# Performance work log

Measured on AMD Instinct MI355X. Metric: run time of the kernel, lower is better.

Reference implementation:

```python
import jax, jax.numpy as jnp
import numpy as np
from jax import lax

B, DIM, DIM_OUT, NH = 8, 512, 512, 8
HD = DIM_OUT // NH          # 64, also the depthwise-conv channel count
SQ, SKV = (1, 1), (2, 2)    # stride_q, stride_kv
PAD = 1                      # kernel 3 -> padding 3//2
SCALE = HD ** -0.5
EPS = 1e-6


def _dw_conv(x, w, stride):
    # x: [N, C, H, W], w: [C, 1, kh, kw]; depthwise conv (groups = C), no bias
    return lax.conv_general_dilated(
        x, w, window_strides=stride, padding=[(PAD, PAD), (PAD, PAD)],
        dimension_numbers=('NCHW', 'OIHW', 'NCHW'),
        feature_group_count=x.shape[1])


def _ln(x, w, b):
    m = jnp.mean(x, -1, keepdims=True)
    v = jnp.var(x, -1, keepdims=True)
    return (x - m) * lax.rsqrt(v + EPS) * w + b


def _pool(t, w, stride, ln_w, ln_b, H, W):
    # t: [B, NH, 1+H*W, HD] with cls token at index 0
    Bn = t.shape[0]
    cls = t[:, :, :1, :]
    body = t[:, :, 1:, :].reshape(Bn * NH, H, W, HD).transpose(0, 3, 1, 2)
    body = _dw_conv(body, w, stride)
    ph, pw = body.shape[2], body.shape[3]
    body = body.reshape(Bn, NH, HD, ph * pw).transpose(0, 1, 3, 2)
    out = jnp.concatenate([cls, body], axis=2)
    return _ln(out, ln_w, ln_b), (ph, pw)


def _rel_bias(r_q4, q_shape, k_shape, rel_pos_h, rel_pos_w):
    # r_q4: [B, NH, q_h*q_w, HD] (cls token stripped)
    q_h, q_w = q_shape
    k_h, k_w = k_shape

    def dist(qs, ks):
        qr, kr = max(ks / qs, 1.0), max(qs / ks, 1.0)
        d = np.arange(qs)[:, None] * qr - np.arange(ks)[None, :] * kr + (ks - 1) * kr
        return d.astype(np.int64)

    Rh = rel_pos_h[dist(q_h, k_h)]  # [q_h, k_h, HD]
    Rw = rel_pos_w[dist(q_w, k_w)]  # [q_w, k_w, HD]
    r_q = r_q4.reshape(r_q4.shape[0], NH, q_h, q_w, HD)
    rel_h = jnp.einsum('byhwc,hkc->byhwk', r_q, Rh)  # [B,NH,q_h,q_w,k_h]
    rel_w = jnp.einsum('byhwc,wkc->byhwk', r_q, Rw)  # [B,NH,q_h,q_w,k_w]
    return rel_h[..., :, None] + rel_w[..., None, :]  # [B,NH,q_h,q_w,k_h,k_w]


def setup_inputs() -> dict:
    key = jax.random.key(0)
    ks = jax.random.split(key, 16)
    H = W = 56
    N = H * W + 1
    rel_dim = 2 * H - 1  # 111
    return {
        'x': jax.random.normal(ks[0], (B, N, DIM), jnp.float32),
        'qkv_w': jax.random.normal(ks[1], (3 * DIM_OUT, DIM), jnp.float32) * DIM ** -0.5,
        'qkv_b': jax.random.normal(ks[2], (3 * DIM_OUT,), jnp.float32) * 0.02,
        'proj_w': jax.random.normal(ks[3], (DIM_OUT, DIM_OUT), jnp.float32) * DIM_OUT ** -0.5,
        'proj_b': jax.random.normal(ks[4], (DIM_OUT,), jnp.float32) * 0.02,
        'pool_q_w': jax.random.normal(ks[5], (HD, 1, 3, 3), jnp.float32) / 3.0,
        'pool_k_w': jax.random.normal(ks[6], (HD, 1, 3, 3), jnp.float32) / 3.0,
        'pool_v_w': jax.random.normal(ks[7], (HD, 1, 3, 3), jnp.float32) / 3.0,
        'lnq_w': 1.0 + 0.1 * jax.random.normal(ks[8], (HD,), jnp.float32),
        'lnq_b': 0.02 * jax.random.normal(ks[9], (HD,), jnp.float32),
        'lnk_w': 1.0 + 0.1 * jax.random.normal(ks[10], (HD,), jnp.float32),
        'lnk_b': 0.02 * jax.random.normal(ks[11], (HD,), jnp.float32),
        'lnv_w': 1.0 + 0.1 * jax.random.normal(ks[12], (HD,), jnp.float32),
        'lnv_b': 0.02 * jax.random.normal(ks[13], (HD,), jnp.float32),
        'rel_pos_h': 0.02 * jax.random.normal(ks[14], (rel_dim, HD), jnp.float32),
        'rel_pos_w': 0.02 * jax.random.normal(ks[15], (rel_dim, HD), jnp.float32),
        'hw_h': 56,
        'hw_w': 56,
    }


def reference(x, qkv_w, qkv_b, proj_w, proj_b, pool_q_w, pool_k_w, pool_v_w,
              lnq_w, lnq_b, lnk_w, lnk_b, lnv_w, lnv_b, rel_pos_h, rel_pos_w,
              hw_h, hw_w):
    Bn, N, _ = x.shape
    qkv = (x @ qkv_w.T + qkv_b).reshape(Bn, N, 3, NH, HD).transpose(2, 0, 3, 1, 4)
    q, k, v = qkv[0], qkv[1], qkv[2]  # each [B, NH, N, HD]
    q, q_shape = _pool(q, pool_q_w, SQ, lnq_w, lnq_b, hw_h, hw_w)
    k, k_shape = _pool(k, pool_k_w, SKV, lnk_w, lnk_b, hw_h, hw_w)
    v, _ = _pool(v, pool_v_w, SKV, lnv_w, lnv_b, hw_h, hw_w)
    attn = (q * SCALE) @ k.swapaxes(-2, -1)  # [B, NH, Nq, Nk]
    q_h, q_w = q_shape
    k_h, k_w = k_shape
    bias = _rel_bias(q[:, :, 1:, :], q_shape, k_shape, rel_pos_h, rel_pos_w)
    blk = attn[:, :, 1:, 1:].reshape(Bn, NH, q_h, q_w, k_h, k_w) + bias
    attn = attn.at[:, :, 1:, 1:].set(blk.reshape(Bn, NH, q_h * q_w, k_h * k_w))
    attn = jax.nn.softmax(attn, axis=-1)
    out = attn @ v                                   # [B, NH, Nq, HD]
    out = out.at[:, :, 1:, :].add(q[:, :, 1:, :])    # residual on non-cls rows
    out = out.transpose(0, 2, 1, 3).reshape(Bn, -1, DIM_OUT)
    return out @ proj_w.T + proj_b
```

## Files before the change

### kernel.cpp

```cpp
#include <hip/hip_runtime.h>
#include <hip/hip_bf16.h>
#include <cstdint>
#include <cstddef>

#define BB 8
#define NHH 8
#define NQ 3137
#define NKV 785
#define HDIM 64
#define AUG 128
#define MROWS (BB*NQ)
#define SCALE 0.125f
#define NKV_PAD 800

typedef unsigned short ushort_t;
typedef __attribute__((ext_vector_type(8))) short s16x8;
typedef __attribute__((ext_vector_type(4))) float f32x4;
typedef __attribute__((ext_vector_type(16))) float f32x16;

__device__ __forceinline__ float bf2f(ushort_t u) {
  union { unsigned int i; float f; } v; v.i = ((unsigned int)u) << 16; return v.f;
}
__device__ __forceinline__ ushort_t f2bf(float f) {
  union { float f; unsigned int i; } v; v.f = f;
  unsigned int r = v.i + 0x7fffu + ((v.i >> 16) & 1u);
  return (ushort_t)(r >> 16);
}
__device__ __forceinline__ unsigned int cvt_pk_bf16(float lo, float hi) {
  unsigned int r;
  asm("v_cvt_pk_bf16_f32 %0, %1, %2" : "=v"(r) : "v"(lo), "v"(hi));
  return r;
}

template<int EPI, bool AF32, bool WF32>
__global__ __launch_bounds__(256) void mfma_gemm_bt(
    const void* __restrict__ Ap, const void* __restrict__ Wp,
    const float* __restrict__ bias, void* __restrict__ outp, int M) {
  __shared__ ushort_t As[128][40];
  __shared__ ushort_t Bs[128][40];
  const int tid = threadIdx.x;
  const int l = tid & 63, w = tid >> 6;
  const int wr = w >> 1, wc = w & 1;
  const int lrow = l & 15, lk = l >> 4;
  const int m0 = blockIdx.y * 128, n0 = blockIdx.x * 128;
  const int srow = tid >> 2, sch = tid & 3;
  const int mA0 = m0 + srow      < M ? m0 + srow      : M - 1;
  const int mA1 = m0 + 64 + srow < M ? m0 + 64 + srow : M - 1;
  const size_t ar0 = (size_t)mA0 * 512, ar1 = (size_t)mA1 * 512;
  const size_t br0 = (size_t)(n0 + srow) * 512, br1 = (size_t)(n0 + 64 + srow) * 512;
  const ushort_t* Ab = (const ushort_t*)Ap;
  const float*    Af = (const float*)Ap;
  const ushort_t* Wb = (const ushort_t*)Wp;
  const float*    Wf = (const float*)Wp;
  auto ld8 = [&](const ushort_t* pb, const float* pf, size_t ofs, bool f32) -> uint4 {
    if (!f32) return *(const uint4*)(pb + ofs);
    const float4 v0 = *(const float4*)(pf + ofs);
    const float4 v1 = *(const float4*)(pf + ofs + 4);
    uint4 r;
    r.x = cvt_pk_bf16(v0.x, v0.y); r.y = cvt_pk_bf16(v0.z, v0.w);
    r.z = cvt_pk_bf16(v1.x, v1.y); r.w = cvt_pk_bf16(v1.z, v1.w);
    return r;
  };
  f32x4 acc[4][4];
  #pragma unroll
  for (int i = 0; i < 4; ++i) {
    #pragma unroll
    for (int j = 0; j < 4; ++j) acc[i][j] = (f32x4){0.f, 0.f, 0.f, 0.f};
  }
  for (int k0 = 0; k0 < 512; k0 += 32) {
    const uint4 a0 = ld8(Ab, Af, ar0 + k0 + sch * 8, AF32);
    const uint4 a1 = ld8(Ab, Af, ar1 + k0 + sch * 8, AF32);
    const uint4 b0 = ld8(Wb, Wf, br0 + k0 + sch * 8, WF32);
    const uint4 b1 = ld8(Wb, Wf, br1 + k0 + sch * 8, WF32);
    __syncthreads();
    *(uint4*)(&As[srow][sch * 8])      = a0;
    *(uint4*)(&As[64 + srow][sch * 8]) = a1;
    *(uint4*)(&Bs[srow][sch * 8])      = b0;
    *(uint4*)(&Bs[64 + srow][sch * 8]) = b1;
    __syncthreads();
    s16x8 af[4], bfr[4];
    #pragma unroll
    for (int mi = 0; mi < 4; ++mi)
      af[mi] = *(const s16x8*)(&As[wr * 64 + mi * 16 + lrow][lk * 8]);
    #pragma unroll
    for (int ni = 0; ni < 4; ++ni)
      bfr[ni] = *(const s16x8*)(&Bs[wc * 64 + ni * 16 + lrow][lk * 8]);
    #pragma unroll
    for (int mi = 0; mi < 4; ++mi) {
      #pragma unroll
      for (int ni = 0; ni < 4; ++ni)
        acc[mi][ni] = __builtin_amdgcn_mfma_f32_16x16x32_bf16(
            af[mi], bfr[ni], acc[mi][ni], 0, 0, 0);
    }
  }
  #pragma unroll
  for (int mi = 0; mi < 4; ++mi) {
    #pragma unroll
    for (int r = 0; r < 4; ++r) {
      const int m = m0 + wr * 64 + mi * 16 + 4 * lk + r;
      if (m >= M) continue;
      #pragma unroll
      for (int ni = 0; ni < 4; ++ni) {
        const int n = n0 + wc * 64 + ni * 16 + lrow;
        const float v = acc[mi][ni][r] + bias[n];
        if (EPI == 0) {
          const int which = n >> 9, y = (n >> 6) & 7, c = n & 63;
          const int b_ = m / NQ, tok = m - b_ * NQ;
          ((ushort_t*)outp)[((((size_t)which * BB + b_) * NHH + y) * NQ + tok) * HDIM + c] = f2bf(v);
        } else {
          ((float*)outp)[(size_t)m * 512 + n] = v;
        }
      }
    }
  }
}

template<int MODE>
__global__ __launch_bounds__(256) void pool_ln_kernel(
    const ushort_t* __restrict__ in, ushort_t* __restrict__ out0,
    ushort_t* __restrict__ out1,
    const float* __restrict__ cw, const float* __restrict__ lnw,
    const float* __restrict__ lnb, int stride, int OW, int R, int Rp) {
  const int tid = threadIdx.x;
  const int c = tid & 63;
  const int rid = blockIdx.x * 4 + (tid >> 6);
  const int by = rid / Rp;
  const int n = rid - by * Rp;
  const bool vrow = (n < R);
  const ushort_t* ibase = in + (size_t)by * NQ * HDIM;
  float val = 0.f;
  if (vrow) {
    if (n == 0) {
      val = bf2f(ibase[c]);
    } else {
      const int p = n - 1;
      const int ho = p / OW, wo = p - ho * OW;
      float s = 0.f;
      #pragma unroll
      for (int dh = 0; dh < 3; ++dh) {
        const int hh = ho * stride + dh - 1;
        if (hh < 0 || hh >= 56) continue;
        #pragma unroll
        for (int dw = 0; dw < 3; ++dw) {
          const int ww = wo * stride + dw - 1;
          if (ww < 0 || ww >= 56) continue;
          s += cw[c * 9 + dh * 3 + dw] * bf2f(ibase[(size_t)(1 + hh * 56 + ww) * HDIM + c]);
        }
      }
      val = s;
    }
  }
  float sum = val, sq = val * val;
  #pragma unroll
  for (int off = 32; off > 0; off >>= 1) {
    sum += __shfl_xor(sum, off);
    sq  += __shfl_xor(sq,  off);
  }
  const float mean = sum * (1.f / 64.f);
  const float var  = sq * (1.f / 64.f) - mean * mean;
  const float rs = rsqrtf(var + 1e-6f);
  const float lno = (val - mean) * rs * lnw[c] + lnb[c];
  if (MODE == 1) {
    out0[(size_t)rid * HDIM + c] = f2bf(lno);
    out1[(size_t)rid * AUG + c] = f2bf(lno * SCALE);
    out1[(size_t)rid * AUG + 64 + c] = 0;
  } else if (MODE == 2) {
    const size_t base = ((size_t)by * 25 + (n >> 5)) * 8;
    const int lf = n & 31;
    {
      const int ch = c;
      const size_t ofs = (base + (ch >> 4)) * 512 +
                         (size_t)(lf | (((ch >> 3) & 1) << 5)) * 8 + (ch & 7);
      out0[ofs] = vrow ? f2bf(lno) : (ushort_t)0;
    }
    {
      const int ch = 64 + c;
      ushort_t aug = 0;
      if (vrow && n >= 1) {
        const int p = n - 1;
        const int kh = p / 28, kw = p - 28 * kh;
        if (c < 28) { if (c == kh) aug = 0x3F80; }
        else if (c < 56) { if (c - 28 == kw) aug = 0x3F80; }
      }
      const size_t ofs = (base + (ch >> 4)) * 512 +
                         (size_t)(lf | (((ch >> 3) & 1) << 5)) * 8 + (ch & 7);
      out0[ofs] = aug;
    }
  } else {
    const size_t ofs = (((size_t)by * 50 + (n >> 4)) * 2 + (c >> 5)) * 512 +
                       (size_t)((c & 31) | (((n >> 3) & 1) << 5)) * 8 + (n & 7);
    out0[ofs] = vrow ? f2bf(lno) : (ushort_t)0;
  }
}

__global__ __launch_bounds__(256) void relbias_mfma_kernel(
    const ushort_t* __restrict__ qb, const float* __restrict__ rph,
    const float* __restrict__ rpw, ushort_t* __restrict__ qaug) {
  const int tid = threadIdx.x;
  const int l = tid & 63, w = tid >> 6;
  const int lrow = l & 15, lk = l >> 4;
  const int hw = blockIdx.y;
  const int mode = blockIdx.z;
  const int r0 = blockIdx.x * 256 + w * 64;
  const float* tab = mode ? rpw : rph;
  s16x8 bfr[2][2];
  #pragma unroll
  for (int ni = 0; ni < 2; ++ni) {
    const int kh = ni * 16 + lrow;
    int trow = hw - 2 * kh + 54;
    if (trow < 0) trow = 0;
    const float* tr = tab + (size_t)trow * 64 + lk * 8;
    #pragma unroll
    for (int k0 = 0; k0 < 2; ++k0) {
      const float4 t0 = *(const float4*)(tr + k0 * 32);
      const float4 t1 = *(const float4*)(tr + k0 * 32 + 4);
      s16x8 bb;
      bb[0] = (short)f2bf(t0.x); bb[1] = (short)f2bf(t0.y);
      bb[2] = (short)f2bf(t0.z); bb[3] = (short)f2bf(t0.w);
      bb[4] = (short)f2bf(t1.x); bb[5] = (short)f2bf(t1.y);
      bb[6] = (short)f2bf(t1.z); bb[7] = (short)f2bf(t1.w);
      bfr[ni][k0] = bb;
    }
  }
  s16x8 af[4][2];
  #pragma unroll
  for (int mi = 0; mi < 4; ++mi) {
    const int rA = r0 + mi * 16 + lrow;
    const int by = rA / 56, oth = rA - 56 * by;
    const int tok = mode ? (1 + oth * 56 + hw) : (1 + hw * 56 + oth);
    const ushort_t* qp = qb + ((size_t)by * NQ + tok) * HDIM + lk * 8;
    af[mi][0] = *(const s16x8*)(qp);
    af[mi][1] = *(const s16x8*)(qp + 32);
  }
  f32x4 acc[4][2];
  #pragma unroll
  for (int mi = 0; mi < 4; ++mi) {
    #pragma unroll
    for (int ni = 0; ni < 2; ++ni) acc[mi][ni] = (f32x4){0.f, 0.f, 0.f, 0.f};
  }
  #pragma unroll
  for (int k0 = 0; k0 < 2; ++k0) {
    #pragma unroll
    for (int mi = 0; mi < 4; ++mi) {
      #pragma unroll
      for (int ni = 0; ni < 2; ++ni)
        acc[mi][ni] = __builtin_amdgcn_mfma_f32_16x16x32_bf16(
            af[mi][k0], bfr[ni][k0], acc[mi][ni], 0, 0, 0);
    }
  }
  const int augofs = 64 + mode * 28;
  #pragma unroll
  for (int mi = 0; mi < 4; ++mi) {
    #pragma unroll
    for (int r = 0; r < 4; ++r) {
      const int row = r0 + mi * 16 + 4 * lk + r;
      const int by = row / 56, oth = row - 56 * by;
      const int tok = 1 + (mode ? (oth * 56 + hw) : (hw * 56 + oth));
      ushort_t* orow = qaug + ((size_t)by * NQ + tok) * AUG + augofs;
      #pragma unroll
      for (int ni = 0; ni < 2; ++ni) {
        const int kh = ni * 16 + lrow;
        if (kh < 28) orow[kh] = f2bf(acc[mi][ni][r]);
      }
    }
  }
}

__global__ __launch_bounds__(256) void attn_mfma32_kernel(
    const ushort_t* __restrict__ qaug, const ushort_t* __restrict__ kfrag,
    const ushort_t* __restrict__ vfrag, const ushort_t* __restrict__ qb,
    ushort_t* __restrict__ outp) {
  const int tid = threadIdx.x;
  const int l = tid & 63;
  const int w = tid >> 6;
  const int h = l >> 5, q5 = l & 31;
  const int by = blockIdx.y;
  const int qt0 = blockIdx.x * 128;
  const int qloc = w * 32 + q5;
  const int qglob = qt0 + qloc;
  const int qcl = qglob < NQ ? qglob : NQ - 1;
  const ushort_t* qrow = qaug + ((size_t)by * NQ + qcl) * AUG;
  s16x8 qf[8];
  #pragma unroll
  for (int cb = 0; cb < 8; ++cb)
    qf[cb] = *(const s16x8*)(qrow + cb * 16 + h * 8);
  f32x16 ot0, ot1;
  #pragma unroll
  for (int i = 0; i < 16; ++i) { ot0[i] = 0.f; ot1[i] = 0.f; }
  float mr = -1e30f, lr = 0.f;
  const ushort_t* kfb = kfrag + (size_t)by * 25 * 8 * 512 + (size_t)l * 8;
  const ushort_t* vfb = vfrag + (size_t)by * 50 * 2 * 512 + (size_t)l * 8;
  #pragma unroll 1
  for (int it = 0; it < 13; ++it) {
    const int jt0 = 2 * it;
    const int jt1 = (2 * it + 1 < 25) ? 2 * it + 1 : 24;
    f32x16 st0, st1;
    #pragma unroll
    for (int i = 0; i < 16; ++i) { st0[i] = 0.f; st1[i] = 0.f; }
    __builtin_amdgcn_s_setprio(1);
    #pragma unroll
    for (int cb = 0; cb < 8; ++cb) {
      const s16x8 kf0 = *(const s16x8*)(kfb + (size_t)(jt0 * 8 + cb) * 512);
      const s16x8 kf1 = *(const s16x8*)(kfb + (size_t)(jt1 * 8 + cb) * 512);
      st0 = __builtin_amdgcn_mfma_f32_32x32x16_bf16(kf0, qf[cb], st0, 0, 0, 0);
      st1 = __builtin_amdgcn_mfma_f32_32x32x16_bf16(kf1, qf[cb], st1, 0, 0, 0);
    }
    __builtin_amdgcn_s_setprio(0);
    if (it == 12) {
      #pragma unroll
      for (int r = 0; r < 16; ++r) {
        const int klocal = (r & 3) + 8 * (r >> 2) + 4 * h;
        if (768 + klocal >= NKV) st0[r] = -1e30f;
        st1[r] = -1e30f;
      }
    }
    float mloc = st0[0];
    #pragma unroll
    for (int r = 1; r < 16; ++r) mloc = fmaxf(mloc, st0[r]);
    #pragma unroll
    for (int r = 0; r < 16; ++r) mloc = fmaxf(mloc, st1[r]);
    mloc = fmaxf(mloc, __shfl_xor(mloc, 32));
    if (!__all(mloc <= mr + 8.f)) {
      const float mn = fmaxf(mr, mloc);
      const float sc = __expf(mr - mn);
      mr = mn;
      lr *= sc;
      #pragma unroll
      for (int i = 0; i < 16; ++i) { ot0[i] *= sc; ot1[i] *= sc; }
    }
    float ps = 0.f;
    #pragma unroll
    for (int r = 0; r < 16; ++r) { st0[r] = __expf(st0[r] - mr); ps += st0[r]; }
    #pragma unroll
    for (int r = 0; r < 16; ++r) { st1[r] = __expf(st1[r] - mr); ps += st1[r]; }
    ps += __shfl_xor(ps, 32);
    lr += ps;
    auto pvstep = [&](const f32x16& pv, int kt) {
      #pragma unroll
      for (int kbk = 0; kbk < 2; ++kbk) {
        const unsigned int pk01 = cvt_pk_bf16(pv[kbk * 8 + 0], pv[kbk * 8 + 1]);
        const unsigned int pk23 = cvt_pk_bf16(pv[kbk * 8 + 2], pv[kbk * 8 + 3]);
        const unsigned int pk45 = cvt_pk_bf16(pv[kbk * 8 + 4], pv[kbk * 8 + 5]);
        const unsigned int pk67 = cvt_pk_bf16(pv[kbk * 8 + 6], pv[kbk * 8 + 7]);
        const unsigned int sA = (unsigned int)__shfl_xor((int)pk01, 32);
        const unsigned int sB = (unsigned int)__shfl_xor((int)pk45, 32);
        const unsigned int sC = (unsigned int)__shfl_xor((int)pk23, 32);
        const unsigned int sD = (unsigned int)__shfl_xor((int)pk67, 32);
        int4 fw;
        fw.x = (int)(h ? sB : pk01);
        fw.y = (int)(h ? sD : pk23);
        fw.z = (int)(h ? pk45 : sA);
        fw.w = (int)(h ? pk67 : sC);
        s16x8 pf;
        __builtin_memcpy(&pf, &fw, 16);
        int g = it * 4 + kt * 2 + kbk;
        if (g > 49) g = 49;
        const s16x8 v0 = *(const s16x8*)(vfb + (size_t)(g * 2 + 0) * 512);
        const s16x8 v1 = *(const s16x8*)(vfb + (size_t)(g * 2 + 1) * 512);
        __builtin_amdgcn_s_setprio(1);
        ot0 = __builtin_amdgcn_mfma_f32_32x32x16_bf16(v0, pf, ot0, 0, 0, 0);
        ot1 = __builtin_amdgcn_mfma_f32_32x32x16_bf16(v1, pf, ot1, 0, 0, 0);
        __builtin_amdgcn_s_setprio(0);
      }
    };
    pvstep(st0, 0);
    pvstep(st1, 1);
  }
  const float inv = 1.f / lr;
  if (qglob < NQ) {
    const int b_ = by >> 3, y_ = by & 7;
    ushort_t* obase = outp + ((size_t)b_ * NQ + qglob) * 512 + (size_t)y_ * 64;
    const ushort_t* rbase = qb + ((size_t)by * NQ + qglob) * HDIM;
    #pragma unroll
    for (int ch = 0; ch < 2; ++ch) {
      #pragma unroll
      for (int rg = 0; rg < 4; ++rg) {
        const int c0 = ch * 32 + 8 * rg + 4 * h;
        float vv[4];
        #pragma unroll
        for (int e = 0; e < 4; ++e)
          vv[e] = (ch ? ot1[rg * 4 + e] : ot0[rg * 4 + e]) * inv;
        if (qglob > 0) {
          #pragma unroll
          for (int e = 0; e < 4; ++e) vv[e] += bf2f(rbase[c0 + e]);
        }
        ushort_t pk[4] = { f2bf(vv[0]), f2bf(vv[1]), f2bf(vv[2]), f2bf(vv[3]) };
        *(uint2*)(obase + c0) = *(const uint2*)pk;
      }
    }
  }
}

extern "C" void kernel_launch(void* const* d_in, const int* in_sizes, int n_in,
                              void* d_out, int out_size, void* d_ws, size_t ws_size,
                              hipStream_t stream) {
  const float* x        = (const float*)d_in[0];
  const float* qkv_w    = (const float*)d_in[1];
  const float* qkv_b    = (const float*)d_in[2];
  const float* proj_w   = (const float*)d_in[3];
  const float* proj_b   = (const float*)d_in[4];
  const float* pool_q_w = (const float*)d_in[5];
  const float* pool_k_w = (const float*)d_in[6];
  const float* pool_v_w = (const float*)d_in[7];
  const float* lnq_w    = (const float*)d_in[8];
  const float* lnq_b    = (const float*)d_in[9];
  const float* lnk_w    = (const float*)d_in[10];
  const float* lnk_b    = (const float*)d_in[11];
  const float* lnv_w    = (const float*)d_in[12];
  const float* lnv_b    = (const float*)d_in[13];
  const float* rel_pos_h = (const float*)d_in[14];
  const float* rel_pos_w = (const float*)d_in[15];

  constexpr size_t E1 = (size_t)BB * NHH * NQ * HDIM;
  char* ws = (char*)d_ws;
  size_t off = 0;
  ushort_t* qkv_raw = (ushort_t*)(ws + off); off += 3 * E1 * 2;
  ushort_t* q_bf    = (ushort_t*)(ws + off); off += E1 * 2;
  ushort_t* qaug    = (ushort_t*)(ws + off); off += (size_t)BB * NHH * NQ * AUG * 2;
  ushort_t* kfrag   = (ushort_t*)(ws + off); off += (size_t)64 * 25 * 8 * 512 * 2;
  ushort_t* vfrag   = (ushort_t*)(ws + off); off += (size_t)64 * 50 * 2 * 512 * 2;
  ushort_t* attn_bf = qkv_raw;

  mfma_gemm_bt<0, true, true><<<dim3(12, 197), 256, 0, stream>>>(
      x, qkv_w, qkv_b, (void*)qkv_raw, MROWS);

  pool_ln_kernel<1><<<(64 * NQ) / 4, 256, 0, stream>>>(
      qkv_raw, q_bf, qaug, pool_q_w, lnq_w, lnq_b, 1, 56, NQ, NQ);
  pool_ln_kernel<2><<<(64 * NKV_PAD) / 4, 256, 0, stream>>>(
      qkv_raw + E1, kfrag, nullptr, pool_k_w, lnk_w, lnk_b, 2, 28, NKV, NKV_PAD);
  pool_ln_kernel<0><<<(64 * NKV_PAD) / 4, 256, 0, stream>>>(
      qkv_raw + 2 * E1, vfrag, nullptr, pool_v_w, lnv_w, lnv_b, 2, 28, NKV, NKV_PAD);

  relbias_mfma_kernel<<<dim3(14, 56, 2), 256, 0, stream>>>(q_bf, rel_pos_h, rel_pos_w, qaug);

  attn_mfma32_kernel<<<dim3(25, 64), 256, 0, stream>>>(qaug, kfrag, vfrag, q_bf, attn_bf);

  mfma_gemm_bt<1, false, true><<<dim3(4, 197), 256, 0, stream>>>(
      attn_bf, proj_w, proj_b, d_out, MROWS);
}
```

Measured before the change: 524.3 us.

## Stage K tiles in swizzled LDS shared across waves in attention kernel

K is now written as plain row-major augmented rows instead of a pre-swizzled MFMA fragment layout. The attention kernel cooperatively loads each 64-key tile into XOR-swizzled LDS once per block and feeds the MFMAs from there, so the four waves no longer each read the same K fragments from global memory. The row max and sum reductions become tree reductions to shorten dependency chains. The cost is two __syncthreads per iteration and LDS traffic. The K pool launch also shrinks to NKV rows, and clamped tail rows are masked anyway.

```diff
diff --git a/kernel.cpp b/kernel.cpp
--- a/kernel.cpp
+++ b/kernel.cpp
@@ -30,6 +30,10 @@
   unsigned int r;
   asm("v_cvt_pk_bf16_f32 %0, %1, %2" : "=v"(r) : "v"(lo), "v"(hi));
   return r;
+}
+__device__ __forceinline__ s16x8 lds_frag16(const ushort_t* base, int row, int slot) {
+  const char* p = (const char*)base + row * 256 + (((slot ^ (row & 15)) & 15) << 4);
+  return *(const s16x8*)p;
 }
 
 template<int EPI, bool AF32, bool WF32>
@@ -165,27 +169,15 @@
     out1[(size_t)rid * AUG + c] = f2bf(lno * SCALE);
     out1[(size_t)rid * AUG + 64 + c] = 0;
   } else if (MODE == 2) {
-    const size_t base = ((size_t)by * 25 + (n >> 5)) * 8;
-    const int lf = n & 31;
-    {
-      const int ch = c;
-      const size_t ofs = (base + (ch >> 4)) * 512 +
-                         (size_t)(lf | (((ch >> 3) & 1) << 5)) * 8 + (ch & 7);
-      out0[ofs] = vrow ? f2bf(lno) : (ushort_t)0;
-    }
-    {
-      const int ch = 64 + c;
-      ushort_t aug = 0;
-      if (vrow && n >= 1) {
-        const int p = n - 1;
-        const int kh = p / 28, kw = p - 28 * kh;
-        if (c < 28) { if (c == kh) aug = 0x3F80; }
-        else if (c < 56) { if (c - 28 == kw) aug = 0x3F80; }
-      }
-      const size_t ofs = (base + (ch >> 4)) * 512 +
-                         (size_t)(lf | (((ch >> 3) & 1) << 5)) * 8 + (ch & 7);
-      out0[ofs] = aug;
-    }
+    out0[(size_t)rid * AUG + c] = f2bf(lno);
+    ushort_t aug = 0;
+    if (n >= 1) {
+      const int p = n - 1;
+      const int kh = p / 28, kw = p - 28 * kh;
+      if (c < 28) { if (c == kh) aug = 0x3F80; }
+      else if (c < 56) { if (c - 28 == kw) aug = 0x3F80; }
+    }
+    out0[(size_t)rid * AUG + 64 + c] = aug;
   } else {
     const size_t ofs = (((size_t)by * 50 + (n >> 4)) * 2 + (c >> 5)) * 512 +
                        (size_t)((c & 31) | (((n >> 3) & 1) << 5)) * 8 + (n & 7);
@@ -267,9 +259,10 @@
 }
 
 __global__ __launch_bounds__(256) void attn_mfma32_kernel(
-    const ushort_t* __restrict__ qaug, const ushort_t* __restrict__ kfrag,
+    const ushort_t* __restrict__ qaug, const ushort_t* __restrict__ kaug,
     const ushort_t* __restrict__ vfrag, const ushort_t* __restrict__ qb,
     ushort_t* __restrict__ outp) {
+  __shared__ ushort_t Kl[64 * AUG];
   const int tid = threadIdx.x;
   const int l = tid & 63;
   const int w = tid >> 6;
@@ -288,22 +281,37 @@
   #pragma unroll
   for (int i = 0; i < 16; ++i) { ot0[i] = 0.f; ot1[i] = 0.f; }
   float mr = -1e30f, lr = 0.f;
-  const ushort_t* kfb = kfrag + (size_t)by * 25 * 8 * 512 + (size_t)l * 8;
+  const int krow = tid >> 2, ks4 = (tid & 3) * 4;
+  const ushort_t* kbase = kaug + (size_t)by * NKV * AUG + ks4 * 8;
   const ushort_t* vfb = vfrag + (size_t)by * 50 * 2 * 512 + (size_t)l * 8;
   #pragma unroll 1
   for (int it = 0; it < 13; ++it) {
-    const int jt0 = 2 * it;
-    const int jt1 = (2 * it + 1 < 25) ? 2 * it + 1 : 24;
+    int jK = it * 64 + krow; if (jK > NKV - 1) jK = NKV - 1;
+    const ushort_t* ksrc = kbase + (size_t)jK * AUG;
+    const uint4 kd0 = *(const uint4*)(ksrc);
+    const uint4 kd1 = *(const uint4*)(ksrc + 8);
+    const uint4 kd2 = *(const uint4*)(ksrc + 16);
+    const uint4 kd3 = *(const uint4*)(ksrc + 24);
+    __syncthreads();
+    {
+      char* kb_ = (char*)Kl + krow * 256;
+      const int rm = krow & 15;
+      *(uint4*)(kb_ + (((ks4 + 0) ^ rm) << 4)) = kd0;
+      *(uint4*)(kb_ + (((ks4 + 1) ^ rm) << 4)) = kd1;
+      *(uint4*)(kb_ + (((ks4 + 2) ^ rm) << 4)) = kd2;
+      *(uint4*)(kb_ + (((ks4 + 3) ^ rm) << 4)) = kd3;
+    }
+    __syncthreads();
     f32x16 st0, st1;
     #pragma unroll
     for (int i = 0; i < 16; ++i) { st0[i] = 0.f; st1[i] = 0.f; }
     __builtin_amdgcn_s_setprio(1);
     #pragma unroll
     for (int cb = 0; cb < 8; ++cb) {
-      const s16x8 kf0 = *(const s16x8*)(kfb + (size_t)(jt0 * 8 + cb) * 512);
-      const s16x8 kf1 = *(const s16x8*)(kfb + (size_t)(jt1 * 8 + cb) * 512);
-      st0 = __builtin_amdgcn_mfma_f32_32x32x16_bf16(kf0, qf[cb], st0, 0, 0, 0);
-      st1 = __builtin_amdgcn_mfma_f32_32x32x16_bf16(kf1, qf[cb], st1, 0, 0, 0);
+      st0 = __builtin_amdgcn_mfma_f32_32x32x16_bf16(
+          lds_frag16(Kl, q5, cb * 2 + h), qf[cb], st0, 0, 0, 0);
+      st1 = __builtin_amdgcn_mfma_f32_32x32x16_bf16(
+          lds_frag16(Kl, 32 + q5, cb * 2 + h), qf[cb], st1, 0, 0, 0);
     }
     __builtin_amdgcn_s_setprio(0);
     if (it == 12) {
@@ -314,12 +322,16 @@
         st1[r] = -1e30f;
       }
     }
-    float mloc = st0[0];
-    #pragma unroll
-    for (int r = 1; r < 16; ++r) mloc = fmaxf(mloc, st0[r]);
-    #pragma unroll
-    for (int r = 0; r < 16; ++r) mloc = fmaxf(mloc, st1[r]);
-    mloc = fmaxf(mloc, __shfl_xor(mloc, 32));
+    float tm[16];
+    #pragma unroll
+    for (int r = 0; r < 16; ++r) tm[r] = fmaxf(st0[r], st1[r]);
+    #pragma unroll
+    for (int s = 8; s > 0; s >>= 1) {
+      #pragma unroll
+      for (int r = 0; r < 8; ++r)
+        if (r < s) tm[r] = fmaxf(tm[r], tm[r + s]);
+    }
+    float mloc = fmaxf(tm[0], __shfl_xor(tm[0], 32));
     if (!__all(mloc <= mr + 8.f)) {
       const float mn = fmaxf(mr, mloc);
       const float sc = __expf(mr - mn);
@@ -328,13 +340,20 @@
       #pragma unroll
       for (int i = 0; i < 16; ++i) { ot0[i] *= sc; ot1[i] *= sc; }
     }
-    float ps = 0.f;
-    #pragma unroll
-    for (int r = 0; r < 16; ++r) { st0[r] = __expf(st0[r] - mr); ps += st0[r]; }
-    #pragma unroll
-    for (int r = 0; r < 16; ++r) { st1[r] = __expf(st1[r] - mr); ps += st1[r]; }
-    ps += __shfl_xor(ps, 32);
-    lr += ps;
+    float ts[16];
+    #pragma unroll
+    for (int r = 0; r < 16; ++r) {
+      st0[r] = __expf(st0[r] - mr);
+      st1[r] = __expf(st1[r] - mr);
+      ts[r] = st0[r] + st1[r];
+    }
+    #pragma unroll
+    for (int s = 8; s > 0; s >>= 1) {
+      #pragma unroll
+      for (int r = 0; r < 8; ++r)
+        if (r < s) ts[r] += ts[r + s];
+    }
+    lr += ts[0] + __shfl_xor(ts[0], 32);
     auto pvstep = [&](const f32x16& pv, int kt) {
       #pragma unroll
       for (int kbk = 0; kbk < 2; ++kbk) {
@@ -417,7 +436,7 @@
   ushort_t* qkv_raw = (ushort_t*)(ws + off); off += 3 * E1 * 2;
   ushort_t* q_bf    = (ushort_t*)(ws + off); off += E1 * 2;
   ushort_t* qaug    = (ushort_t*)(ws + off); off += (size_t)BB * NHH * NQ * AUG * 2;
-  ushort_t* kfrag   = (ushort_t*)(ws + off); off += (size_t)64 * 25 * 8 * 512 * 2;
+  ushort_t* kaug    = (ushort_t*)(ws + off); off += (size_t)BB * NHH * NKV * AUG * 2;
   ushort_t* vfrag   = (ushort_t*)(ws + off); off += (size_t)64 * 50 * 2 * 512 * 2;
   ushort_t* attn_bf = qkv_raw;
 
@@ -426,14 +445,14 @@
 
   pool_ln_kernel<1><<<(64 * NQ) / 4, 256, 0, stream>>>(
       qkv_raw, q_bf, qaug, pool_q_w, lnq_w, lnq_b, 1, 56, NQ, NQ);
-  pool_ln_kernel<2><<<(64 * NKV_PAD) / 4, 256, 0, stream>>>(
-      qkv_raw + E1, kfrag, nullptr, pool_k_w, lnk_w, lnk_b, 2, 28, NKV, NKV_PAD);
+  pool_ln_kernel<2><<<(64 * NKV) / 4, 256, 0, stream>>>(
+      qkv_raw + E1, kaug, nullptr, pool_k_w, lnk_w, lnk_b, 2, 28, NKV, NKV);
   pool_ln_kernel<0><<<(64 * NKV_PAD) / 4, 256, 0, stream>>>(
       qkv_raw + 2 * E1, vfrag, nullptr, pool_v_w, lnv_w, lnv_b, 2, 28, NKV, NKV_PAD);
 
   relbias_mfma_kernel<<<dim3(14, 56, 2), 256, 0, stream>>>(q_bf, rel_pos_h, rel_pos_w, qaug);
 
-  attn_mfma32_kernel<<<dim3(25, 64), 256, 0, stream>>>(qaug, kfrag, vfrag, q_bf, attn_bf);
+  attn_mfma32_kernel<<<dim3(25, 64), 256, 0, stream>>>(qaug, kaug, vfrag, q_bf, attn_bf);
 
   mfma_gemm_bt<1, false, true><<<dim3(4, 197), 256, 0, stream>>>(
       attn_bf, proj_w, proj_b, d_out, MROWS);
```

Result: faster. 479.7 us (-8.5%).

## Stage K/V fragments in LDS for attention and widen GEMM K-tile

Applied to the files above, without the earlier changes.

The attention kernel now cooperatively loads each iteration's K and V fragment tiles into shared memory once per block, so the four waves no longer each fetch them from global memory. To support this, K/V padding grows to 832 rows so every tile is full, and the clamping of tile indices is removed. The GEMM K-step is doubled to 64 with a wider LDS tile, which halves the number of barriers. The row-sum and row-max reductions are rewritten as trees. The cost is extra LDS traffic and barriers inside the attention loop, plus larger workspace buffers.

```diff
diff --git a/kernel.cpp b/kernel.cpp
--- a/kernel.cpp
+++ b/kernel.cpp
@@ -11,7 +11,7 @@
 #define AUG 128
 #define MROWS (BB*NQ)
 #define SCALE 0.125f
-#define NKV_PAD 800
+#define NKV_PAD 832
 
 typedef unsigned short ushort_t;
 typedef __attribute__((ext_vector_type(8))) short s16x8;
@@ -36,18 +36,17 @@
 __global__ __launch_bounds__(256) void mfma_gemm_bt(
     const void* __restrict__ Ap, const void* __restrict__ Wp,
     const float* __restrict__ bias, void* __restrict__ outp, int M) {
-  __shared__ ushort_t As[128][40];
-  __shared__ ushort_t Bs[128][40];
+  __shared__ ushort_t As[128][72];
+  __shared__ ushort_t Bs[128][72];
   const int tid = threadIdx.x;
   const int l = tid & 63, w = tid >> 6;
   const int wr = w >> 1, wc = w & 1;
   const int lrow = l & 15, lk = l >> 4;
   const int m0 = blockIdx.y * 128, n0 = blockIdx.x * 128;
-  const int srow = tid >> 2, sch = tid & 3;
-  const int mA0 = m0 + srow      < M ? m0 + srow      : M - 1;
-  const int mA1 = m0 + 64 + srow < M ? m0 + 64 + srow : M - 1;
-  const size_t ar0 = (size_t)mA0 * 512, ar1 = (size_t)mA1 * 512;
-  const size_t br0 = (size_t)(n0 + srow) * 512, br1 = (size_t)(n0 + 64 + srow) * 512;
+  const int srow = tid >> 1, sh = (tid & 1) * 32;
+  const int mA = m0 + srow < M ? m0 + srow : M - 1;
+  const size_t ar = (size_t)mA * 512 + sh;
+  const size_t br = (size_t)(n0 + srow) * 512 + sh;
   const ushort_t* Ab = (const ushort_t*)Ap;
   const float*    Af = (const float*)Ap;
   const ushort_t* Wb = (const ushort_t*)Wp;
@@ -67,30 +66,35 @@
     #pragma unroll
     for (int j = 0; j < 4; ++j) acc[i][j] = (f32x4){0.f, 0.f, 0.f, 0.f};
   }
-  for (int k0 = 0; k0 < 512; k0 += 32) {
-    const uint4 a0 = ld8(Ab, Af, ar0 + k0 + sch * 8, AF32);
-    const uint4 a1 = ld8(Ab, Af, ar1 + k0 + sch * 8, AF32);
-    const uint4 b0 = ld8(Wb, Wf, br0 + k0 + sch * 8, WF32);
-    const uint4 b1 = ld8(Wb, Wf, br1 + k0 + sch * 8, WF32);
+  for (int k0 = 0; k0 < 512; k0 += 64) {
+    uint4 a[4], b[4];
+    #pragma unroll
+    for (int j = 0; j < 4; ++j) a[j] = ld8(Ab, Af, ar + k0 + j * 8, AF32);
+    #pragma unroll
+    for (int j = 0; j < 4; ++j) b[j] = ld8(Wb, Wf, br + k0 + j * 8, WF32);
     __syncthreads();
-    *(uint4*)(&As[srow][sch * 8])      = a0;
-    *(uint4*)(&As[64 + srow][sch * 8]) = a1;
-    *(uint4*)(&Bs[srow][sch * 8])      = b0;
-    *(uint4*)(&Bs[64 + srow][sch * 8]) = b1;
+    #pragma unroll
+    for (int j = 0; j < 4; ++j) {
+      *(uint4*)(&As[srow][sh + j * 8]) = a[j];
+      *(uint4*)(&Bs[srow][sh + j * 8]) = b[j];
+    }
     __syncthreads();
-    s16x8 af[4], bfr[4];
-    #pragma unroll
-    for (int mi = 0; mi < 4; ++mi)
-      af[mi] = *(const s16x8*)(&As[wr * 64 + mi * 16 + lrow][lk * 8]);
-    #pragma unroll
-    for (int ni = 0; ni < 4; ++ni)
-      bfr[ni] = *(const s16x8*)(&Bs[wc * 64 + ni * 16 + lrow][lk * 8]);
-    #pragma unroll
-    for (int mi = 0; mi < 4; ++mi) {
+    #pragma unroll
+    for (int sub = 0; sub < 2; ++sub) {
+      s16x8 af[4], bfr[4];
+      #pragma unroll
+      for (int mi = 0; mi < 4; ++mi)
+        af[mi] = *(const s16x8*)(&As[wr * 64 + mi * 16 + lrow][sub * 32 + lk * 8]);
       #pragma unroll
       for (int ni = 0; ni < 4; ++ni)
-        acc[mi][ni] = __builtin_amdgcn_mfma_f32_16x16x32_bf16(
-            af[mi], bfr[ni], acc[mi][ni], 0, 0, 0);
+        bfr[ni] = *(const s16x8*)(&Bs[wc * 64 + ni * 16 + lrow][sub * 32 + lk * 8]);
+      #pragma unroll
+      for (int mi = 0; mi < 4; ++mi) {
+        #pragma unroll
+        for (int ni = 0; ni < 4; ++ni)
+          acc[mi][ni] = __builtin_amdgcn_mfma_f32_16x16x32_bf16(
+              af[mi], bfr[ni], acc[mi][ni], 0, 0, 0);
+      }
     }
   }
   #pragma unroll
@@ -165,7 +169,7 @@
     out1[(size_t)rid * AUG + c] = f2bf(lno * SCALE);
     out1[(size_t)rid * AUG + 64 + c] = 0;
   } else if (MODE == 2) {
-    const size_t base = ((size_t)by * 25 + (n >> 5)) * 8;
+    const size_t base = ((size_t)by * 26 + (n >> 5)) * 8;
     const int lf = n & 31;
     {
       const int ch = c;
@@ -187,7 +191,7 @@
       out0[ofs] = aug;
     }
   } else {
-    const size_t ofs = (((size_t)by * 50 + (n >> 4)) * 2 + (c >> 5)) * 512 +
+    const size_t ofs = (((size_t)by * 52 + (n >> 4)) * 2 + (c >> 5)) * 512 +
                        (size_t)((c & 31) | (((n >> 3) & 1) << 5)) * 8 + (n & 7);
     out0[ofs] = vrow ? f2bf(lno) : (ushort_t)0;
   }
@@ -270,6 +274,8 @@
     const ushort_t* __restrict__ qaug, const ushort_t* __restrict__ kfrag,
     const ushort_t* __restrict__ vfrag, const ushort_t* __restrict__ qb,
     ushort_t* __restrict__ outp) {
+  __shared__ ushort_t Kl[16 * 512];
+  __shared__ ushort_t Vl[8 * 512];
   const int tid = threadIdx.x;
   const int l = tid & 63;
   const int w = tid >> 6;
@@ -288,22 +294,37 @@
   #pragma unroll
   for (int i = 0; i < 16; ++i) { ot0[i] = 0.f; ot1[i] = 0.f; }
   float mr = -1e30f, lr = 0.f;
-  const ushort_t* kfb = kfrag + (size_t)by * 25 * 8 * 512 + (size_t)l * 8;
-  const ushort_t* vfb = vfrag + (size_t)by * 50 * 2 * 512 + (size_t)l * 8;
+  const ushort_t* kfb = kfrag + (size_t)by * 26 * 8 * 512;
+  const ushort_t* vfb = vfrag + (size_t)by * 52 * 2 * 512;
   #pragma unroll 1
   for (int it = 0; it < 13; ++it) {
-    const int jt0 = 2 * it;
-    const int jt1 = (2 * it + 1 < 25) ? 2 * it + 1 : 24;
+    const ushort_t* ksrc = kfb + (size_t)it * 16 * 512;
+    const ushort_t* vsrc = vfb + (size_t)it * 8 * 512;
+    uint4 ks[4], vs[2];
+    #pragma unroll
+    for (int j = 0; j < 4; ++j)
+      ks[j] = *(const uint4*)(ksrc + (size_t)(j * 256 + tid) * 8);
+    #pragma unroll
+    for (int j = 0; j < 2; ++j)
+      vs[j] = *(const uint4*)(vsrc + (size_t)(j * 256 + tid) * 8);
+    __syncthreads();
+    #pragma unroll
+    for (int j = 0; j < 4; ++j)
+      *(uint4*)(Kl + (size_t)(j * 256 + tid) * 8) = ks[j];
+    #pragma unroll
+    for (int j = 0; j < 2; ++j)
+      *(uint4*)(Vl + (size_t)(j * 256 + tid) * 8) = vs[j];
+    __syncthreads();
     f32x16 st0, st1;
     #pragma unroll
     for (int i = 0; i < 16; ++i) { st0[i] = 0.f; st1[i] = 0.f; }
     __builtin_amdgcn_s_setprio(1);
     #pragma unroll
     for (int cb = 0; cb < 8; ++cb) {
-      const s16x8 kf0 = *(const s16x8*)(kfb + (size_t)(jt0 * 8 + cb) * 512);
-      const s16x8 kf1 = *(const s16x8*)(kfb + (size_t)(jt1 * 8 + cb) * 512);
-      st0 = __builtin_amdgcn_mfma_f32_32x32x16_bf16(kf0, qf[cb], st0, 0, 0, 0);
-      st1 = __builtin_amdgcn_mfma_f32_32x32x16_bf16(kf1, qf[cb], st1, 0, 0, 0);
+      const s16x8 k0f = *(const s16x8*)(Kl + (size_t)cb * 512 + (size_t)l * 8);
+      const s16x8 k1f = *(const s16x8*)(Kl + (size_t)(8 + cb) * 512 + (size_t)l * 8);
+      st0 = __builtin_amdgcn_mfma_f32_32x32x16_bf16(k0f, qf[cb], st0, 0, 0, 0);
+      st1 = __builtin_amdgcn_mfma_f32_32x32x16_bf16(k1f, qf[cb], st1, 0, 0, 0);
     }
     __builtin_amdgcn_s_setprio(0);
     if (it == 12) {
@@ -314,12 +335,16 @@
         st1[r] = -1e30f;
       }
     }
-    float mloc = st0[0];
-    #pragma unroll
-    for (int r = 1; r < 16; ++r) mloc = fmaxf(mloc, st0[r]);
-    #pragma unroll
-    for (int r = 0; r < 16; ++r) mloc = fmaxf(mloc, st1[r]);
-    mloc = fmaxf(mloc, __shfl_xor(mloc, 32));
+    float tm[16];
+    #pragma unroll
+    for (int r = 0; r < 16; ++r) tm[r] = fmaxf(st0[r], st1[r]);
+    #pragma unroll
+    for (int s = 8; s > 0; s >>= 1) {
+      #pragma unroll
+      for (int r = 0; r < 8; ++r)
+        if (r < s) tm[r] = fmaxf(tm[r], tm[r + s]);
+    }
+    float mloc = fmaxf(tm[0], __shfl_xor(tm[0], 32));
     if (!__all(mloc <= mr + 8.f)) {
       const float mn = fmaxf(mr, mloc);
       const float sc = __expf(mr - mn);
@@ -328,13 +353,20 @@
       #pragma unroll
       for (int i = 0; i < 16; ++i) { ot0[i] *= sc; ot1[i] *= sc; }
     }
-    float ps = 0.f;
-    #pragma unroll
-    for (int r = 0; r < 16; ++r) { st0[r] = __expf(st0[r] - mr); ps += st0[r]; }
-    #pragma unroll
-    for (int r = 0; r < 16; ++r) { st1[r] = __expf(st1[r] - mr); ps += st1[r]; }
-    ps += __shfl_xor(ps, 32);
-    lr += ps;
+    float ts[16];
+    #pragma unroll
+    for (int r = 0; r < 16; ++r) {
+      st0[r] = __expf(st0[r] - mr);
+      st1[r] = __expf(st1[r] - mr);
+      ts[r] = st0[r] + st1[r];
+    }
+    #pragma unroll
+    for (int s = 8; s > 0; s >>= 1) {
+      #pragma unroll
+      for (int r = 0; r < 8; ++r)
+        if (r < s) ts[r] += ts[r + s];
+    }
+    lr += ts[0] + __shfl_xor(ts[0], 32);
     auto pvstep = [&](const f32x16& pv, int kt) {
       #pragma unroll
       for (int kbk = 0; kbk < 2; ++kbk) {
@@ -353,10 +385,9 @@
         fw.w = (int)(h ? pk67 : sC);
         s16x8 pf;
         __builtin_memcpy(&pf, &fw, 16);
-        int g = it * 4 + kt * 2 + kbk;
-        if (g > 49) g = 49;
-        const s16x8 v0 = *(const s16x8*)(vfb + (size_t)(g * 2 + 0) * 512);
-        const s16x8 v1 = *(const s16x8*)(vfb + (size_t)(g * 2 + 1) * 512);
+        const int fb = (kt * 2 + kbk) * 2;
+        const s16x8 v0 = *(const s16x8*)(Vl + (size_t)(fb + 0) * 512 + (size_t)l * 8);
+        const s16x8 v1 = *(const s16x8*)(Vl + (size_t)(fb + 1) * 512 + (size_t)l * 8);
         __builtin_amdgcn_s_setprio(1);
         ot0 = __builtin_amdgcn_mfma_f32_32x32x16_bf16(v0, pf, ot0, 0, 0, 0);
         ot1 = __builtin_amdgcn_mfma_f32_32x32x16_bf16(v1, pf, ot1, 0, 0, 0);
@@ -417,8 +448,8 @@
   ushort_t* qkv_raw = (ushort_t*)(ws + off); off += 3 * E1 * 2;
   ushort_t* q_bf    = (ushort_t*)(ws + off); off += E1 * 2;
   ushort_t* qaug    = (ushort_t*)(ws + off); off += (size_t)BB * NHH * NQ * AUG * 2;
-  ushort_t* kfrag   = (ushort_t*)(ws + off); off += (size_t)64 * 25 * 8 * 512 * 2;
-  ushort_t* vfrag   = (ushort_t*)(ws + off); off += (size_t)64 * 50 * 2 * 512 * 2;
+  ushort_t* kfrag   = (ushort_t*)(ws + off); off += (size_t)64 * 26 * 8 * 512 * 2;
+  ushort_t* vfrag   = (ushort_t*)(ws + off); off += (size_t)64 * 52 * 2 * 512 * 2;
   ushort_t* attn_bf = qkv_raw;
 
   mfma_gemm_bt<0, true, true><<<dim3(12, 197), 256, 0, stream>>>(
```

Measured after the change: 633.7 us. +20.9%, slower.
